# Kernel optimization log

Measured on AMD Instinct MI355X. Metric: run time of the kernel, lower is better.

The kernel has to match this reference:

```python
import jax, jax.numpy as jnp
import numpy as np

N = 100000      # nodes
E = 3200000     # edges (avg degree 32)
F_IN = 128      # node_features
H1, H2 = 32, 16 # GConvGRU hidden sizes
C = 10          # num_classes
K = 5           # Chebyshev order


def setup_inputs() -> dict:
    key = jax.random.key(0)
    ks = jax.random.split(key, 16)
    s = 0.05
    return {
        "x": jax.random.normal(ks[0], (N, F_IN), jnp.float32),
        "edge_weight": jax.random.uniform(ks[1], (E,), jnp.float32),
        "Wx1": jax.random.normal(ks[2], (3, K, F_IN, H1), jnp.float32) * s,
        "Wh1": jax.random.normal(ks[3], (3, K, H1, H1), jnp.float32) * s,
        "bx1": jax.random.normal(ks[4], (3, H1), jnp.float32) * s,
        "bh1": jax.random.normal(ks[5], (3, H1), jnp.float32) * s,
        "Wx2": jax.random.normal(ks[6], (3, K, H1, H2), jnp.float32) * s,
        "Wh2": jax.random.normal(ks[7], (3, K, H2, H2), jnp.float32) * s,
        "bx2": jax.random.normal(ks[8], (3, H2), jnp.float32) * s,
        "bh2": jax.random.normal(ks[9], (3, H2), jnp.float32) * s,
        "Wlin": jax.random.normal(ks[10], (H2, C), jnp.float32) * s,
        "blin": jax.random.normal(ks[11], (C,), jnp.float32) * s,
        "edge_index": jax.random.randint(ks[12], (2, E), 0, N),
    }


def _cheb_norm(edge_index, edge_weight, n):
    # PyG ChebConv __norm__ with sym normalization and lambda_max=2.0:
    # L_hat = 2/lambda_max * (I - D^-1/2 A D^-1/2) - I = -D^-1/2 A D^-1/2
    row, col = edge_index[0], edge_index[1]
    deg = jax.ops.segment_sum(edge_weight, row, num_segments=n)
    dinv = jnp.where(deg > 0, jax.lax.rsqrt(jnp.where(deg > 0, deg, 1.0)), 0.0)
    norm = -edge_weight * dinv[row] * dinv[col]
    return row, col, norm


def _cheb_conv(x, row, col, norm, W, b, n):
    # Tx_0 = x; Tx_1 = L_hat x; Tx_k = 2 L_hat Tx_{k-1} - Tx_{k-2}
    def spmm(t):
        return jax.ops.segment_sum(norm[:, None] * t[row], col, num_segments=n)
    Tx0 = x
    out = Tx0 @ W[0]
    Tx1 = spmm(Tx0)
    out = out + Tx1 @ W[1]
    for k in range(2, W.shape[0]):
        Tx2 = 2.0 * spmm(Tx1) - Tx0
        out = out + Tx2 @ W[k]
        Tx0, Tx1 = Tx1, Tx2
    return out + b


def _gconv_gru(x, row, col, norm, Wx, Wh, bx, bh, n, hidden):
    h = jnp.zeros((n, hidden), x.dtype)  # H=None -> zeros
    z = jax.nn.sigmoid(_cheb_conv(x, row, col, norm, Wx[0], bx[0], n)
                       + _cheb_conv(h, row, col, norm, Wh[0], bh[0], n))
    r = jax.nn.sigmoid(_cheb_conv(x, row, col, norm, Wx[1], bx[1], n)
                       + _cheb_conv(h, row, col, norm, Wh[1], bh[1], n))
    h_tilde = jnp.tanh(_cheb_conv(x, row, col, norm, Wx[2], bx[2], n)
                       + _cheb_conv(h * r, row, col, norm, Wh[2], bh[2], n))
    return z * h + (1.0 - z) * h_tilde


def reference(x, edge_weight, Wx1, Wh1, bx1, bh1, Wx2, Wh2, bx2, bh2,
              Wlin, blin, edge_index):
    n = x.shape[0]
    row, col, norm = _cheb_norm(edge_index, edge_weight, n)
    h = _gconv_gru(x, row, col, norm, Wx1, Wh1, bx1, bh1, n, H1)
    h = jax.nn.relu(h)  # dropout is identity in eval mode
    h = _gconv_gru(h, row, col, norm, Wx2, Wh2, bx2, bh2, n, H2)
    h = jax.nn.relu(h)
    logits = h @ Wlin + blin
    return jax.nn.log_softmax(logits, axis=1)
```

## Files before the change

kernel.cpp:

```cpp
#include <hip/hip_runtime.h>
#include <hip/hip_fp16.h>
#include <cstdint>

#define N_NODES 100000
#define N_EDGES 3200000
#define RNP 100096
#define SLOTS 80
#define NBUCK 391
#define BCAP 9216
#define BIN_BLOCKS 1024
#define CHUNK 3125

typedef unsigned char uchar;
typedef __attribute__((ext_vector_type(8))) short bf16x8;
typedef __attribute__((ext_vector_type(4))) float f32x4;

__device__ __forceinline__ ushort f2bf(float f) {
  uint u = __float_as_uint(f);
  return (ushort)((u + 0x7FFFu + ((u >> 16) & 1u)) >> 16);
}


__device__ __forceinline__ float fp8d(uint b) {
#if __has_builtin(__builtin_amdgcn_cvt_f32_fp8)
  return __builtin_amdgcn_cvt_f32_fp8((int)b, 0);
#else
  uint em = b & 0x7Fu;
  uint e = em >> 3, m = em & 7u;
  float v = (em >= 8u) ? __uint_as_float(((e + 120u) << 23) | (m << 20)) : 0.f;
  return (b & 0x80u) ? -v : v;
#endif
}

__device__ __forceinline__ uint fp8e(float f) {
#if __has_builtin(__builtin_amdgcn_cvt_pk_fp8_f32)
  return (uint)(__builtin_amdgcn_cvt_pk_fp8_f32(f, f, 0, false) & 0xFF);
#else
  uint u = __float_as_uint(f);
  uint s = (u >> 24) & 0x80u;
  uint au = u & 0x7FFFFFFFu;
  if (au > 0x43E00000u) au = 0x43E00000u;
  au += 0x7FFFFu + ((au >> 20) & 1u);
  uint e = au >> 23;
  uint m = (au >> 20) & 7u;
  int ee = (int)e - 120;
  uint byte = (ee <= 0) ? 0u : (((uint)ee << 3) | m);
  return byte | s;
#endif
}


__global__ __launch_bounds__(256) void k_binR(const int* __restrict__ ei,
    const float* __restrict__ w, int* __restrict__ bcnt, int2* __restrict__ binned) {
  __shared__ int cntL[NBUCK], lstart[NBUCK], gb[NBUCK], lofs[NBUCK];
  __shared__ int2 staged[CHUNK];
  __shared__ ushort bid[CHUNK];
  int t = threadIdx.x;
  int e0 = blockIdx.x * CHUNK;
  for (int i = t; i < NBUCK; i += 256) cntL[i] = 0;
  __syncthreads();
  for (int j = t; j < CHUNK; j += 256) {
    int r = ei[e0 + j];
    atomicAdd(&cntL[r >> 8], 1);
  }
  __syncthreads();
  if (t == 0) {
    int run = 0;
    for (int b = 0; b < NBUCK; ++b) { lstart[b] = run; run += cntL[b]; }
  }
  __syncthreads();
  for (int b = t; b < NBUCK; b += 256) {
    lofs[b] = lstart[b];
    gb[b] = cntL[b] ? atomicAdd(&bcnt[b], cntL[b]) : 0;
  }
  __syncthreads();
  for (int j = t; j < CHUNK; j += 256) {
    int r = ei[e0 + j];
    float we = w[e0 + j];
    int b = r >> 8;
    int pos = atomicAdd(&lofs[b], 1);
    staged[pos] = make_int2(r & 255, __float_as_int(we));
    bid[pos] = (ushort)b;
  }
  __syncthreads();
  for (int i = t; i < CHUNK; i += 256) {
    int b = bid[i];
    binned[(size_t)b * BCAP + gb[b] + (i - lstart[b])] = staged[i];
  }
}


__global__ __launch_bounds__(256) void k_degw(const int* __restrict__ bcnt,
    const int2* __restrict__ binned, float* __restrict__ dinv) {
  __shared__ float acc[256];
  int b = blockIdx.x, t = threadIdx.x;
  acc[t] = 0.f;
  __syncthreads();
  int n = bcnt[b];
  const int2* seg = binned + (size_t)b * BCAP;
  for (int i = t; i < n; i += 256) {
    int2 q = seg[i];
    atomicAdd(&acc[q.x], __int_as_float(q.y));
  }
  __syncthreads();
  int node = b * 256 + t;
  if (node < N_NODES) {
    float d = acc[t];
    dinv[node] = d > 0.f ? rsqrtf(d) : 0.f;
  }
}


__global__ __launch_bounds__(256) void k_binD(const int* __restrict__ ei,
    const float* __restrict__ w, const float* __restrict__ dinv,
    int* __restrict__ bcnt, int2* __restrict__ binned) {
  __shared__ int cntL[NBUCK], lstart[NBUCK], gb[NBUCK], lofs[NBUCK];
  __shared__ int2 staged[CHUNK];
  __shared__ ushort bid[CHUNK];
  int t = threadIdx.x;
  int e0 = blockIdx.x * CHUNK;
  for (int i = t; i < NBUCK; i += 256) cntL[i] = 0;
  __syncthreads();
  for (int j = t; j < CHUNK; j += 256) {
    int c = ei[N_EDGES + e0 + j];
    atomicAdd(&cntL[c >> 8], 1);
  }
  __syncthreads();
  if (t == 0) {
    int run = 0;
    for (int b = 0; b < NBUCK; ++b) { lstart[b] = run; run += cntL[b]; }
  }
  __syncthreads();
  for (int b = t; b < NBUCK; b += 256) {
    lofs[b] = lstart[b];
    gb[b] = cntL[b] ? atomicAdd(&bcnt[b], cntL[b]) : 0;
  }
  __syncthreads();
  for (int j = t; j < CHUNK; j += 256) {
    int r = ei[e0 + j], c = ei[N_EDGES + e0 + j];
    float v = w[e0 + j] * dinv[r];
    int b = c >> 8;
    int pos = atomicAdd(&lofs[b], 1);
    staged[pos] = make_int2((r << 8) | (c & 255), __float_as_int(v));
    bid[pos] = (ushort)b;
  }
  __syncthreads();
  for (int i = t; i < CHUNK; i += 256) {
    int b = bid[i];
    binned[(size_t)b * BCAP + gb[b] + (i - lstart[b])] = staged[i];
  }
}


__global__ __launch_bounds__(256) void k_ell(const int* __restrict__ bcnt,
    const int2* __restrict__ binned, const float* __restrict__ dinv,
    int* __restrict__ cnt, int* __restrict__ packed) {
  __shared__ int lofs[256];
  __shared__ float dloc[256];
  int b = blockIdx.x, t = threadIdx.x;
  lofs[t] = 0;
  int node = b * 256 + t;
  dloc[t] = node < N_NODES ? dinv[node] : 0.f;
  __syncthreads();
  int n = bcnt[b];
  const int2* seg = binned + (size_t)b * BCAP;
  for (int i = t; i < n; i += 256) {
    int2 q = seg[i];
    int cl = q.x & 255;
    uint r = (uint)q.x >> 8;
    float v = -__int_as_float(q.y) * dloc[cl];
    int pos = atomicAdd(&lofs[cl], 1);
    if (pos < SLOTS)
      packed[(size_t)(b * 256 + cl) * SLOTS + pos] =
          (int)((r << 14) | fp8e(v * 256.f));
  }
  __syncthreads();
  if (node < N_NODES) {
    int cn = min(lofs[t], SLOTS);
    int cnR = min((cn + 15) & ~15, SLOTS);
    size_t base = (size_t)node * SLOTS;
    for (int s = cn; s < cnR; ++s) packed[base + s] = 0;
    cnt[node] = cn;
  }
}


__global__ __launch_bounds__(256) void k_gemmL1(const float* __restrict__ X,
    const float* __restrict__ Wx1, __half* __restrict__ P, uchar* __restrict__ P8) {
  __shared__ ushort As[128][136];
  __shared__ ushort Bs[64][136];
  int t = threadIdx.x;
  int wv = t >> 6, l = t & 63;
  int nodeBase = blockIdx.x * 128;
  #pragma unroll 4
  for (int it = 0; it < 16; ++it) {
    int idx = it * 256 + t;
    int nn = idx >> 5, c4 = idx & 31;
    int node = nodeBase + nn;
    float4 v = make_float4(0.f, 0.f, 0.f, 0.f);
    if (node < N_NODES) v = *(const float4*)(X + (size_t)node * 128 + c4 * 4);
    ushort4 b4;
    b4.x = f2bf(v.x); b4.y = f2bf(v.y); b4.z = f2bf(v.z); b4.w = f2bf(v.w);
    *(ushort4*)&As[nn][c4 * 4] = b4;
  }
  __syncthreads();
  bf16x8 afr[2][4];
  #pragma unroll
  for (int rf = 0; rf < 2; ++rf) {
    int row = wv * 32 + rf * 16 + (l & 15);
    #pragma unroll
    for (int s = 0; s < 4; ++s)
      afr[rf][s] = *(const bf16x8*)&As[row][s * 32 + (l >> 4) * 8];
  }
  for (int k = 0; k < 5; ++k) {
    const float* Wz = Wx1 + (size_t)k * 4096;
    const float* Wh = Wx1 + (size_t)(10 + k) * 4096;
    __syncthreads();
    for (int idx = t; idx < 4096; idx += 256) {
      int kk = idx >> 5, c = idx & 31;
      Bs[c][kk]      = f2bf(Wz[idx]);
      Bs[c + 32][kk] = f2bf(Wh[idx]);
    }
    __syncthreads();
    __half* Pk = P + (size_t)k * N_NODES * 64;
    #pragma unroll
    for (int cf = 0; cf < 4; ++cf) {
      f32x4 acc0 = {0.f, 0.f, 0.f, 0.f};
      f32x4 acc1 = {0.f, 0.f, 0.f, 0.f};
      #pragma unroll
      for (int s = 0; s < 4; ++s) {
        bf16x8 bfr = *(const bf16x8*)&Bs[cf * 16 + (l & 15)][s * 32 + (l >> 4) * 8];
        acc0 = __builtin_amdgcn_mfma_f32_16x16x32_bf16(afr[0][s], bfr, acc0, 0, 0, 0);
        acc1 = __builtin_amdgcn_mfma_f32_16x16x32_bf16(afr[1][s], bfr, acc1, 0, 0, 0);
      }
      int col = cf * 16 + (l & 15);
      #pragma unroll
      for (int r = 0; r < 4; ++r) {
        int n0 = nodeBase + wv * 32 + (l >> 4) * 4 + r;
        if (n0 < N_NODES) {
          Pk[(size_t)n0 * 64 + col] = __float2half_rn(acc0[r]);
          if (k == 4) P8[(size_t)n0 * 64 + col] = (uchar)fp8e(acc0[r]);
        }
        if (n0 + 16 < N_NODES) {
          Pk[(size_t)(n0 + 16) * 64 + col] = __float2half_rn(acc1[r]);
          if (k == 4) P8[(size_t)(n0 + 16) * 64 + col] = (uchar)fp8e(acc1[r]);
        }
      }
    }
  }
}


__global__ __launch_bounds__(256) void k_gemm5_L2(const __half* __restrict__ Hin,
    const float* __restrict__ Wx2, __half* __restrict__ P, uchar* __restrict__ P8) {
  __shared__ float xs[128][34];
  __shared__ float wsh[5][32][32];
  int t = threadIdx.x;
  int nodeBase = blockIdx.x * 128;
  for (int idx = t; idx < 128 * 4; idx += 256) {
    int nn = idx >> 2, q = idx & 3;
    int node = nodeBase + nn;
    float v[8] = {0.f, 0.f, 0.f, 0.f, 0.f, 0.f, 0.f, 0.f};
    if (node < N_NODES) {
      int4 raw = *(const int4*)(Hin + (size_t)node * 32 + q * 8);
      const __half2* hp = (const __half2*)&raw;
      #pragma unroll
      for (int j = 0; j < 4; ++j) {
        float2 f = __half22float2(hp[j]);
        v[2 * j] = f.x; v[2 * j + 1] = f.y;
      }
    }
    #pragma unroll
    for (int j = 0; j < 8; ++j) xs[nn][q * 8 + j] = v[j];
  }
  for (int idx = t; idx < 5 * 512; idx += 256) {
    int k = idx / 512, rem = idx % 512;
    int kk = rem >> 4, c = rem & 15;
    wsh[k][kk][c]      = Wx2[(size_t)k * 512 + rem];
    wsh[k][kk][c + 16] = Wx2[(size_t)(10 + k) * 512 + rem];
  }
  __syncthreads();
  int cg = t & 7, ng = t >> 3;
  for (int k = 0; k < 5; ++k) {
    float acc[4][4] = {};
    #pragma unroll
    for (int kk = 0; kk < 32; ++kk) {
      float4 wv = *(const float4*)&wsh[k][kk][cg * 4];
      #pragma unroll
      for (int i = 0; i < 4; ++i) {
        float xv = xs[ng * 4 + i][kk];
        acc[i][0] = fmaf(xv, wv.x, acc[i][0]);
        acc[i][1] = fmaf(xv, wv.y, acc[i][1]);
        acc[i][2] = fmaf(xv, wv.z, acc[i][2]);
        acc[i][3] = fmaf(xv, wv.w, acc[i][3]);
      }
    }
    __half* Pk = P + (size_t)k * N_NODES * 32;
    #pragma unroll
    for (int i = 0; i < 4; ++i) {
      int node = nodeBase + ng * 4 + i;
      if (node >= N_NODES) continue;
      size_t o = (size_t)node * 32 + cg * 4;
      *(__half2*)(Pk + o)     = __floats2half2_rn(acc[i][0], acc[i][1]);
      *(__half2*)(Pk + o + 2) = __floats2half2_rn(acc[i][2], acc[i][3]);
      if (k == 4) {
        uint b0 = fp8e(acc[i][0]), b1 = fp8e(acc[i][1]);
        uint b2 = fp8e(acc[i][2]), b3 = fp8e(acc[i][3]);
        *(uint*)(P8 + o) = b0 | (b1 << 8) | (b2 << 16) | (b3 << 24);
      }
    }
  }
}


template <int FINAL>
__global__ __launch_bounds__(256) void k_spmm64(const int* __restrict__ cnt,
    const int* __restrict__ packed, const uchar* __restrict__ B8cur,
    const __half* __restrict__ Pk, const __half* __restrict__ Bprev,
    __half* __restrict__ Bnext, uchar* __restrict__ B8next,
    __half* __restrict__ Hout, const float* __restrict__ bx,
    const float* __restrict__ bh, float scale) {
  int node = blockIdx.x * 4 + (threadIdx.x >> 6);
  uint lane = threadIdx.x & 63;
  if (node >= N_NODES) return;
  int cn = min(cnt[node], SLOTS);
  int cnR = min((cn + 15) & ~15, SLOTS);
  const int* ep = packed + (size_t)node * SLOTS;
  float acc = 0.f;
  for (int i = 0; i < cnR; i += 8) {
    int4 p03 = *(const int4*)(ep + i);
    int4 p47 = *(const int4*)(ep + i + 4);
    float b0 = fp8d(B8cur[((uint)p03.x >> 8) + lane]);
    float b1 = fp8d(B8cur[((uint)p03.y >> 8) + lane]);
    float b2 = fp8d(B8cur[((uint)p03.z >> 8) + lane]);
    float b3 = fp8d(B8cur[((uint)p03.w >> 8) + lane]);
    float b4 = fp8d(B8cur[((uint)p47.x >> 8) + lane]);
    float b5 = fp8d(B8cur[((uint)p47.y >> 8) + lane]);
    float b6 = fp8d(B8cur[((uint)p47.z >> 8) + lane]);
    float b7 = fp8d(B8cur[((uint)p47.w >> 8) + lane]);
    acc = fmaf(fp8d((uint)p03.x & 0xFFu), b0, acc);
    acc = fmaf(fp8d((uint)p03.y & 0xFFu), b1, acc);
    acc = fmaf(fp8d((uint)p03.z & 0xFFu), b2, acc);
    acc = fmaf(fp8d((uint)p03.w & 0xFFu), b3, acc);
    acc = fmaf(fp8d((uint)p47.x & 0xFFu), b4, acc);
    acc = fmaf(fp8d((uint)p47.y & 0xFFu), b5, acc);
    acc = fmaf(fp8d((uint)p47.z & 0xFFu), b6, acc);
    acc = fmaf(fp8d((uint)p47.w & 0xFFu), b7, acc);
  }
  uint no = (uint)node * 64 + lane;
  float F = __half2float(Pk[no]) + scale * acc;
  if (Bprev) F -= __half2float(Bprev[no]);
  if (!FINAL) {
    Bnext[no] = __float2half_rn(F);
    B8next[no] = (uchar)fp8e(F);
  } else {
    float Fp = __shfl_xor(F, 32);
    if (lane < 32) {
      float zb = bx[lane] + bh[lane];
      float hb = bx[64 + lane] + bh[64 + lane];
      float z  = 1.f / (1.f + expf(-(F + zb)));
      float ht = tanhf(Fp + hb);
      float h  = (1.f - z) * ht;
      Hout[(uint)node * 32 + lane] = __float2half_rn(h > 0.f ? h : 0.f);
    }
  }
}


template <int FINAL>
__global__ __launch_bounds__(256) void k_spmm32(const int* __restrict__ cnt,
    const int* __restrict__ packed, const uchar* __restrict__ B8cur,
    const __half* __restrict__ Pk, const __half* __restrict__ Bprev,
    __half* __restrict__ Bnext, uchar* __restrict__ B8next,
    float* __restrict__ Hout, const float* __restrict__ bx,
    const float* __restrict__ bh, float scale) {
  int node = blockIdx.x * 4 + (threadIdx.x >> 6);
  uint lane = threadIdx.x & 63;
  if (node >= N_NODES) return;
  int cn = min(cnt[node], SLOTS);
  int cnR = min((cn + 15) & ~15, SLOTS);
  const int* ep = packed + (size_t)node * SLOTS;
  uint hf = lane >> 5, f = lane & 31;
  float acc = 0.f;
  for (int i = 0; i < cnR; i += 16) {
    int off = i + hf * 8;
    int4 p03 = *(const int4*)(ep + off);
    int4 p47 = *(const int4*)(ep + off + 4);
    float b0 = fp8d(B8cur[((uint)p03.x >> 9) + f]);
    float b1 = fp8d(B8cur[((uint)p03.y >> 9) + f]);
    float b2 = fp8d(B8cur[((uint)p03.z >> 9) + f]);
    float b3 = fp8d(B8cur[((uint)p03.w >> 9) + f]);
    float b4 = fp8d(B8cur[((uint)p47.x >> 9) + f]);
    float b5 = fp8d(B8cur[((uint)p47.y >> 9) + f]);
    float b6 = fp8d(B8cur[((uint)p47.z >> 9) + f]);
    float b7 = fp8d(B8cur[((uint)p47.w >> 9) + f]);
    acc = fmaf(fp8d((uint)p03.x & 0xFFu), b0, acc);
    acc = fmaf(fp8d((uint)p03.y & 0xFFu), b1, acc);
    acc = fmaf(fp8d((uint)p03.z & 0xFFu), b2, acc);
    acc = fmaf(fp8d((uint)p03.w & 0xFFu), b3, acc);
    acc = fmaf(fp8d((uint)p47.x & 0xFFu), b4, acc);
    acc = fmaf(fp8d((uint)p47.y & 0xFFu), b5, acc);
    acc = fmaf(fp8d((uint)p47.z & 0xFFu), b6, acc);
    acc = fmaf(fp8d((uint)p47.w & 0xFFu), b7, acc);
  }
  acc += __shfl_xor(acc, 32);
  uint no = (uint)node * 32 + f;
  float F = __half2float(Pk[no]) + scale * acc;
  if (Bprev) F -= __half2float(Bprev[no]);
  if (!FINAL) {
    if (hf == 0) {
      Bnext[no] = __float2half_rn(F);
      B8next[no] = (uchar)fp8e(F);
    }
  } else {
    float Fp = __shfl_xor(F, 16);
    if (lane < 16) {
      float zb = bx[f] + bh[f];
      float hb = bx[32 + f] + bh[32 + f];
      float z  = 1.f / (1.f + expf(-(F + zb)));
      float ht = tanhf(Fp + hb);
      float h  = (1.f - z) * ht;
      Hout[(uint)node * 16 + f] = h > 0.f ? h : 0.f;
    }
  }
}


__global__ __launch_bounds__(256) void k_head(const float* __restrict__ h,
    const float* __restrict__ Wlin, const float* __restrict__ blin,
    float* __restrict__ out) {
  __shared__ float w[160];
  __shared__ float b[10];
  int t = threadIdx.x;
  if (t < 160) w[t] = Wlin[t];
  if (t < 10)  b[t] = blin[t];
  __syncthreads();
  int node = blockIdx.x * 256 + t;
  if (node >= N_NODES) return;
  float hv[16];
  const float4* hp = (const float4*)(h + (size_t)node * 16);
  #pragma unroll
  for (int q = 0; q < 4; ++q) {
    float4 v = hp[q];
    hv[q * 4 + 0] = v.x; hv[q * 4 + 1] = v.y; hv[q * 4 + 2] = v.z; hv[q * 4 + 3] = v.w;
  }
  float l[10];
  #pragma unroll
  for (int c = 0; c < 10; ++c) {
    float a = b[c];
    #pragma unroll
    for (int j = 0; j < 16; ++j) a = fmaf(hv[j], w[j * 10 + c], a);
    l[c] = a;
  }
  float m = l[0];
  #pragma unroll
  for (int c = 1; c < 10; ++c) m = fmaxf(m, l[c]);
  float ssum = 0.f;
  #pragma unroll
  for (int c = 0; c < 10; ++c) ssum += expf(l[c] - m);
  float lse = m + logf(ssum);
  #pragma unroll
  for (int c = 0; c < 10; ++c) out[(size_t)node * 10 + c] = l[c] - lse;
}


extern "C" void kernel_launch(void* const* d_in, const int* in_sizes, int n_in,
                              void* d_out, int out_size, void* d_ws, size_t ws_size,
                              hipStream_t stream) {
  (void)in_sizes; (void)n_in; (void)out_size; (void)ws_size;
  const float* x    = (const float*)d_in[0];
  const float* ew   = (const float*)d_in[1];
  const float* Wx1  = (const float*)d_in[2];
  const float* bx1  = (const float*)d_in[4];
  const float* bh1  = (const float*)d_in[5];
  const float* Wx2  = (const float*)d_in[6];
  const float* bx2  = (const float*)d_in[8];
  const float* bh2  = (const float*)d_in[9];
  const float* Wlin = (const float*)d_in[10];
  const float* blin = (const float*)d_in[11];
  const int*   ei   = (const int*)d_in[12];
  float* out = (float*)d_out;

  float* ws_f = (float*)d_ws;
  size_t o = 0;
  float*  dinv  = ws_f + o;          o += RNP;
  int*    cnt   = (int*)(ws_f + o);  o += RNP;
  int*    bcntR = (int*)(ws_f + o);  o += 512;
  int*    bcntD = (int*)(ws_f + o);  o += 512;
  float*  regA  = ws_f + o;          o += (size_t)N_NODES * SLOTS;
  float*  regB  = ws_f + o;          o += (size_t)5 * N_NODES * 32;
  __half* BB0   = (__half*)(ws_f + o); o += (size_t)N_NODES * 32;
  __half* BB1   = (__half*)(ws_f + o); o += (size_t)N_NODES * 32;
  __half* BB2   = (__half*)(ws_f + o); o += (size_t)N_NODES * 32;
  uchar*  B8_0  = (uchar*)(ws_f + o);  o += (size_t)N_NODES * 16;
  uchar*  B8_1  = (uchar*)(ws_f + o);  o += (size_t)N_NODES * 16;
  uchar*  B8_2  = (uchar*)(ws_f + o);  o += (size_t)N_NODES * 16;
  uchar*  P8    = (uchar*)(ws_f + o);  o += (size_t)N_NODES * 16;
  __half* h1h   = (__half*)(ws_f + o); o += (size_t)N_NODES * 16;
  float*  h2r   = ws_f + o;          o += (size_t)N_NODES * 16;

  int*    packed  = (int*)regA;
  int2*   binnedR = (int2*)regA;
  int2*   binnedD = (int2*)regB;
  __half* P       = (__half*)regB;

  hipMemsetAsync(bcntR, 0, 1024 * sizeof(int), stream);

  k_binR<<<BIN_BLOCKS, 256, 0, stream>>>(ei, ew, bcntR, binnedR);
  k_degw<<<NBUCK, 256, 0, stream>>>(bcntR, binnedR, dinv);
  k_binD<<<BIN_BLOCKS, 256, 0, stream>>>(ei, ew, dinv, bcntD, binnedD);
  k_ell<<<NBUCK, 256, 0, stream>>>(bcntD, binnedD, dinv, cnt, packed);

  const int SPB = (N_NODES + 3) / 4;
  const float s2 = 2.f / 256.f, s1 = 1.f / 256.f;

  __half* P1[5];
  for (int k = 0; k < 5; ++k) P1[k] = P + (size_t)k * N_NODES * 64;
  k_gemmL1<<<(N_NODES + 127) / 128, 256, 0, stream>>>(x, Wx1, P, P8);
  k_spmm64<0><<<SPB, 256, 0, stream>>>(cnt, packed, P8,   P1[3], nullptr, BB0, B8_0, nullptr, bx1, bh1, s2);
  k_spmm64<0><<<SPB, 256, 0, stream>>>(cnt, packed, B8_0, P1[2], P1[4],   BB1, B8_1, nullptr, bx1, bh1, s2);
  k_spmm64<0><<<SPB, 256, 0, stream>>>(cnt, packed, B8_1, P1[1], BB0,     BB2, B8_2, nullptr, bx1, bh1, s2);
  k_spmm64<1><<<SPB, 256, 0, stream>>>(cnt, packed, B8_2, P1[0], BB1, nullptr, nullptr, h1h, bx1, bh1, s1);

  __half* P2[5];
  for (int k = 0; k < 5; ++k) P2[k] = P + (size_t)k * N_NODES * 32;
  k_gemm5_L2<<<(N_NODES + 127) / 128, 256, 0, stream>>>(h1h, Wx2, P, P8);
  k_spmm32<0><<<SPB, 256, 0, stream>>>(cnt, packed, P8,   P2[3], nullptr, BB0, B8_0, nullptr, bx2, bh2, s2);
  k_spmm32<0><<<SPB, 256, 0, stream>>>(cnt, packed, B8_0, P2[2], P2[4],   BB1, B8_1, nullptr, bx2, bh2, s2);
  k_spmm32<0><<<SPB, 256, 0, stream>>>(cnt, packed, B8_1, P2[1], BB0,     BB2, B8_2, nullptr, bx2, bh2, s2);
  k_spmm32<1><<<SPB, 256, 0, stream>>>(cnt, packed, B8_2, P2[0], BB1, nullptr, nullptr, h2r, bx2, bh2, s1);

  k_head<<<(N_NODES + 255) / 256, 256, 0, stream>>>(h2r, Wlin, blin, out);
}
```

Baseline: 729.8 us.

## Split layer-1 64-column SpMM into two 32-column half passes with edge-split lanes

Each layer-1 SpMM step is split into two launches, each covering 32 of the 64 feature columns. Within a wavefront the two half-waves process alternate 8-edge groups and combine their partial sums with a cross-lane shuffle. The final step stores the z pre-activation to a new fp16 buffer, which the second half pass reads back to compute the gated output. The goal is to shrink each pass's gathered working set so it fits better in cache, at the price of twice the launches, re-reading the edge list twice, and idle lanes during the stores.

```diff
diff --git a/kernel.cpp b/kernel.cpp
--- a/kernel.cpp
+++ b/kernel.cpp
@@ -313,31 +313,34 @@
 }
 
 
-template <int FINAL>
-__global__ __launch_bounds__(256) void k_spmm64(const int* __restrict__ cnt,
+template <int HALF, int FINAL>
+__global__ __launch_bounds__(256) void k_spmm64h(const int* __restrict__ cnt,
     const int* __restrict__ packed, const uchar* __restrict__ B8cur,
     const __half* __restrict__ Pk, const __half* __restrict__ Bprev,
     __half* __restrict__ Bnext, uchar* __restrict__ B8next,
-    __half* __restrict__ Hout, const float* __restrict__ bx,
-    const float* __restrict__ bh, float scale) {
+    __half* __restrict__ Fz, __half* __restrict__ Hout,
+    const float* __restrict__ bx, const float* __restrict__ bh, float scale) {
   int node = blockIdx.x * 4 + (threadIdx.x >> 6);
   uint lane = threadIdx.x & 63;
   if (node >= N_NODES) return;
   int cn = min(cnt[node], SLOTS);
   int cnR = min((cn + 15) & ~15, SLOTS);
   const int* ep = packed + (size_t)node * SLOTS;
+  uint hf = lane >> 5, f = lane & 31;
+  uint colOff = HALF * 32 + f;
   float acc = 0.f;
-  for (int i = 0; i < cnR; i += 8) {
-    int4 p03 = *(const int4*)(ep + i);
-    int4 p47 = *(const int4*)(ep + i + 4);
-    float b0 = fp8d(B8cur[((uint)p03.x >> 8) + lane]);
-    float b1 = fp8d(B8cur[((uint)p03.y >> 8) + lane]);
-    float b2 = fp8d(B8cur[((uint)p03.z >> 8) + lane]);
-    float b3 = fp8d(B8cur[((uint)p03.w >> 8) + lane]);
-    float b4 = fp8d(B8cur[((uint)p47.x >> 8) + lane]);
-    float b5 = fp8d(B8cur[((uint)p47.y >> 8) + lane]);
-    float b6 = fp8d(B8cur[((uint)p47.z >> 8) + lane]);
-    float b7 = fp8d(B8cur[((uint)p47.w >> 8) + lane]);
+  for (int i = 0; i < cnR; i += 16) {
+    int off = i + hf * 8;
+    int4 p03 = *(const int4*)(ep + off);
+    int4 p47 = *(const int4*)(ep + off + 4);
+    float b0 = fp8d(B8cur[((uint)p03.x >> 8) + colOff]);
+    float b1 = fp8d(B8cur[((uint)p03.y >> 8) + colOff]);
+    float b2 = fp8d(B8cur[((uint)p03.z >> 8) + colOff]);
+    float b3 = fp8d(B8cur[((uint)p03.w >> 8) + colOff]);
+    float b4 = fp8d(B8cur[((uint)p47.x >> 8) + colOff]);
+    float b5 = fp8d(B8cur[((uint)p47.y >> 8) + colOff]);
+    float b6 = fp8d(B8cur[((uint)p47.z >> 8) + colOff]);
+    float b7 = fp8d(B8cur[((uint)p47.w >> 8) + colOff]);
     acc = fmaf(fp8d((uint)p03.x & 0xFFu), b0, acc);
     acc = fmaf(fp8d((uint)p03.y & 0xFFu), b1, acc);
     acc = fmaf(fp8d((uint)p03.z & 0xFFu), b2, acc);
@@ -347,21 +350,25 @@
     acc = fmaf(fp8d((uint)p47.z & 0xFFu), b6, acc);
     acc = fmaf(fp8d((uint)p47.w & 0xFFu), b7, acc);
   }
-  uint no = (uint)node * 64 + lane;
+  acc += __shfl_xor(acc, 32);
+  uint no = (uint)node * 64 + colOff;
   float F = __half2float(Pk[no]) + scale * acc;
   if (Bprev) F -= __half2float(Bprev[no]);
   if (!FINAL) {
-    Bnext[no] = __float2half_rn(F);
-    B8next[no] = (uchar)fp8e(F);
+    if (hf == 0) {
+      Bnext[no] = __float2half_rn(F);
+      B8next[no] = (uchar)fp8e(F);
+    }
+  } else if (HALF == 0) {
+    if (hf == 0) Fz[(uint)node * 32 + f] = __float2half_rn(F);
   } else {
-    float Fp = __shfl_xor(F, 32);
-    if (lane < 32) {
-      float zb = bx[lane] + bh[lane];
-      float hb = bx[64 + lane] + bh[64 + lane];
-      float z  = 1.f / (1.f + expf(-(F + zb)));
-      float ht = tanhf(Fp + hb);
+    if (hf == 0) {
+      float zv = __half2float(Fz[(uint)node * 32 + f]) + bx[f] + bh[f];
+      float hv = F + bx[64 + f] + bh[64 + f];
+      float z  = 1.f / (1.f + expf(-zv));
+      float ht = tanhf(hv);
       float h  = (1.f - z) * ht;
-      Hout[(uint)node * 32 + lane] = __float2half_rn(h > 0.f ? h : 0.f);
+      Hout[(uint)node * 32 + f] = __float2half_rn(h > 0.f ? h : 0.f);
     }
   }
 }
@@ -496,6 +503,7 @@
   uchar*  B8_1  = (uchar*)(ws_f + o);  o += (size_t)N_NODES * 16;
   uchar*  B8_2  = (uchar*)(ws_f + o);  o += (size_t)N_NODES * 16;
   uchar*  P8    = (uchar*)(ws_f + o);  o += (size_t)N_NODES * 16;
+  __half* Fz    = (__half*)(ws_f + o); o += (size_t)N_NODES * 16;
   __half* h1h   = (__half*)(ws_f + o); o += (size_t)N_NODES * 16;
   float*  h2r   = ws_f + o;          o += (size_t)N_NODES * 16;
 
@@ -517,10 +525,14 @@
   __half* P1[5];
   for (int k = 0; k < 5; ++k) P1[k] = P + (size_t)k * N_NODES * 64;
   k_gemmL1<<<(N_NODES + 127) / 128, 256, 0, stream>>>(x, Wx1, P, P8);
-  k_spmm64<0><<<SPB, 256, 0, stream>>>(cnt, packed, P8,   P1[3], nullptr, BB0, B8_0, nullptr, bx1, bh1, s2);
-  k_spmm64<0><<<SPB, 256, 0, stream>>>(cnt, packed, B8_0, P1[2], P1[4],   BB1, B8_1, nullptr, bx1, bh1, s2);
-  k_spmm64<0><<<SPB, 256, 0, stream>>>(cnt, packed, B8_1, P1[1], BB0,     BB2, B8_2, nullptr, bx1, bh1, s2);
-  k_spmm64<1><<<SPB, 256, 0, stream>>>(cnt, packed, B8_2, P1[0], BB1, nullptr, nullptr, h1h, bx1, bh1, s1);
+  k_spmm64h<0,0><<<SPB, 256, 0, stream>>>(cnt, packed, P8,   P1[3], nullptr, BB0, B8_0, nullptr, nullptr, bx1, bh1, s2);
+  k_spmm64h<1,0><<<SPB, 256, 0, stream>>>(cnt, packed, P8,   P1[3], nullptr, BB0, B8_0, nullptr, nullptr, bx1, bh1, s2);
+  k_spmm64h<0,0><<<SPB, 256, 0, stream>>>(cnt, packed, B8_0, P1[2], P1[4],   BB1, B8_1, nullptr, nullptr, bx1, bh1, s2);
+  k_spmm64h<1,0><<<SPB, 256, 0, stream>>>(cnt, packed, B8_0, P1[2], P1[4],   BB1, B8_1, nullptr, nullptr, bx1, bh1, s2);
+  k_spmm64h<0,0><<<SPB, 256, 0, stream>>>(cnt, packed, B8_1, P1[1], BB0,     BB2, B8_2, nullptr, nullptr, bx1, bh1, s2);
+  k_spmm64h<1,0><<<SPB, 256, 0, stream>>>(cnt, packed, B8_1, P1[1], BB0,     BB2, B8_2, nullptr, nullptr, bx1, bh1, s2);
+  k_spmm64h<0,1><<<SPB, 256, 0, stream>>>(cnt, packed, B8_2, P1[0], BB1, nullptr, nullptr, Fz, nullptr, bx1, bh1, s1);
+  k_spmm64h<1,1><<<SPB, 256, 0, stream>>>(cnt, packed, B8_2, P1[0], BB1, nullptr, nullptr, Fz, h1h,    bx1, bh1, s1);
 
   __half* P2[5];
   for (int k = 0; k < 5; ++k) P2[k] = P + (size_t)k * N_NODES * 32;
```

Result: slower. 829.3 us (+13.6%).
